# Optimization experiments

Hardware: AMD Instinct MI355X
Metric: run time of the kernel (lower is better)

Reference implementation:

```python
import jax, jax.numpy as jnp
import numpy as np

N_NODES = 25000
N_EDGES = 500000
ND, ED, G = 32, 19, 200


def _lrelu(x):
    return jax.nn.leaky_relu(x, 0.01)


def setup_inputs() -> dict:
    key = jax.random.key(0)
    ks = jax.random.split(key, 12)
    s = 0.05
    return {
        "node_feats": jax.random.normal(ks[0], (N_NODES, ND), jnp.float32),
        "edge_feats": jax.random.normal(ks[1], (N_EDGES, ED), jnp.float32),
        "src": jax.random.randint(ks[2], (N_EDGES,), 0, N_NODES),
        "dst": jax.random.randint(ks[3], (N_EDGES,), 0, N_NODES),
        "Wn": jax.random.normal(ks[4], (G, ND), jnp.float32) * s,
        "bn": jnp.zeros((G,), jnp.float32),
        "We1": jax.random.normal(ks[5], (G, ND + ED), jnp.float32) * s,
        "be1": jnp.zeros((G,), jnp.float32),
        "We2": jax.random.normal(ks[6], (1, 2 * G), jnp.float32) * s,
        "be2": jnp.zeros((1,), jnp.float32),
        "Wet": jax.random.normal(ks[7], (G, G), jnp.float32) * s,
        "bet": jnp.zeros((G,), jnp.float32),
        "W_ih": jax.random.normal(ks[8], (3 * G, G), jnp.float32) * s,
        "b_ih": jnp.zeros((3 * G,), jnp.float32),
        "W_hh": jax.random.normal(ks[9], (3 * G, G), jnp.float32) * s,
        "b_hh": jnp.zeros((3 * G,), jnp.float32),
    }


def reference(node_feats, edge_feats, src, dst, Wn, bn, We1, be1, We2, be2,
              Wet, bet, W_ih, b_ih, W_hh, b_hh):
    N = node_feats.shape[0]
    # project_node: Linear + LeakyReLU -> hv_new [N, G]
    hv_new = _lrelu(node_feats @ Wn.T + bn)
    # apply_edges1 + project_edge1: cat([src hv, he]) -> he1 [E, G]
    he1 = _lrelu(jnp.concatenate([node_feats[src], edge_feats], axis=1) @ We1.T + be1)
    # apply_edges2 + project_edge2: cat([dst hv_new, he1]) -> logits [E, 1]
    he2 = jnp.concatenate([hv_new[dst], he1], axis=1)
    logits = _lrelu(he2 @ We2.T + be2)[:, 0]  # [E]
    # edge_softmax: softmax over incoming edges per destination node
    m = jax.ops.segment_max(logits, dst, num_segments=N)  # [N]
    ex = jnp.exp(logits - m[dst])
    denom = jax.ops.segment_sum(ex, dst, num_segments=N)  # [N]
    a = ex / denom[dst]  # [E]
    # AttentiveGRU1: e = a * edge_transform(he1); scatter-sum to dst
    e = a[:, None] * (he1 @ Wet.T + bet)  # [E, G]
    c = jax.ops.segment_sum(e, dst, num_segments=N)  # [N, G]
    context = jax.nn.elu(c)
    # GRUCell(context, hv_new)
    gi = context @ W_ih.T + b_ih
    gh = hv_new @ W_hh.T + b_hh
    ir, iz, inn = jnp.split(gi, 3, axis=1)
    hr, hz, hn = jnp.split(gh, 3, axis=1)
    r = jax.nn.sigmoid(ir + hr)
    z = jax.nn.sigmoid(iz + hz)
    n = jnp.tanh(inn + r * hn)
    h = (1.0 - z) * n + z * hv_new
    return jax.nn.relu(h)
```

## Files before the change

kernel.cpp:

```cpp
#include <hip/hip_runtime.h>
#include <hip/hip_bf16.h>

#define G 200
#define NDIM 32
#define EDIM 19
#define KIN 51

typedef unsigned short u16;
typedef unsigned int u32;
typedef unsigned long long u64;

typedef __attribute__((ext_vector_type(8))) short bfrag;
typedef __attribute__((ext_vector_type(4))) float ffrag;

__device__ __forceinline__ float lrelu(float x){ return x > 0.f ? x : 0.01f*x; }
__device__ __forceinline__ u16 f2b(float x){ u32 u = __float_as_uint(x); return (u16)((u + 0x7fffu + ((u >> 16) & 1u)) >> 16); }
__device__ __forceinline__ float b2f(u16 x){ return __uint_as_float(((u32)x) << 16); }

#define MFMA16(a, b, c) __builtin_amdgcn_mfma_f32_16x16x32_bf16(a, b, c, 0, 0, 0)

__global__ void zero_kernel(float* __restrict__ s_raw, float* __restrict__ denom,
                            int* __restrict__ deg, float* __restrict__ l1,
                            const float* __restrict__ nf, u16* __restrict__ nfb, int N){
  int i = blockIdx.x * 256 + threadIdx.x;
  if (i < N * G) s_raw[i] = 0.f;
  if (i < N){ denom[i] = 0.f; deg[i] = 0; l1[i] = 0.f; }
  if (i < N * NDIM) nfb[i] = f2b(nf[i]);
}

__global__ void prep_all_kernel(const float* __restrict__ We1, const float* __restrict__ Wn,
                                const float* __restrict__ Wet, const float* __restrict__ Wih,
                                const float* __restrict__ Whh,
                                u16* __restrict__ Wbg, u16* __restrict__ Wnb, u16* __restrict__ Wet2,
                                u16* __restrict__ Wrz, u16* __restrict__ Winn, u16* __restrict__ Whn){
  int idx = blockIdx.x * 256 + threadIdx.x;
  const int s0 = 208 * 64, s1 = 256 * 64, s2 = 208 * 224, s3 = 2 * 208 * 416, s4 = 208 * 224, s5 = 208 * 224;
  if (idx < s0){
    int r = idx >> 6, k = idx & 63;
    Wbg[idx] = f2b((r < G && k < KIN) ? We1[r * KIN + k] : 0.f);
    return;
  }
  idx -= s0;
  if (idx < s1){
    int r = idx >> 6, k = idx & 63;
    Wnb[idx] = f2b((r < G && k < NDIM) ? Wn[r * NDIM + k] : 0.f);
    return;
  }
  idx -= s1;
  if (idx < s2){
    int r = idx / 224, k = idx % 224;
    Wet2[idx] = f2b((r < G && k < G) ? Wet[r * G + k] : 0.f);
    return;
  }
  idx -= s2;
  if (idx < s3){
    int g = idx / (208 * 416), rem = idx % (208 * 416);
    int r = rem / 416, k = rem % 416;
    float v = 0.f;
    if (r < G){
      int row = g * G + r;
      if (k < G) v = Wih[row * G + k];
      else if (k >= 208 && k < 408) v = Whh[row * G + (k - 208)];
    }
    Wrz[idx] = f2b(v);
    return;
  }
  idx -= s3;
  if (idx < s4){
    int r = idx / 224, k = idx % 224;
    Winn[idx] = f2b((r < G && k < G) ? Wih[(2 * G + r) * G + k] : 0.f);
    return;
  }
  idx -= s4;
  if (idx < s5){
    int r = idx / 224, kk = idx % 224;
    Whn[idx] = f2b((r < G && kk >= 16 && kk < 216) ? Whh[(2 * G + r) * G + (kk - 16)] : 0.f);
  }
}

__global__ void deghist_kernel(const int* __restrict__ dst, int* __restrict__ deg, int E){
  int e = blockIdx.x * 256 + threadIdx.x;
  if (e < E) atomicAdd(&deg[dst[e]], 1);
}

__global__ __launch_bounds__(1024) void scan_kernel(const int* __restrict__ deg, int* __restrict__ offs,
                                                    int* __restrict__ cur, int N){
  __shared__ int wsums[16];
  const int C = 25;
  int tid = threadIdx.x;
  int lane = tid & 63, wid = tid >> 6;
  int base = tid * C;
  int loc[C];
  int s = 0;
  #pragma unroll
  for (int i = 0; i < C; ++i){
    int v = (base + i < N) ? deg[base + i] : 0;
    loc[i] = s; s += v;
  }
  int x = s;
  #pragma unroll
  for (int off = 1; off < 64; off <<= 1){
    int y = __shfl_up(x, off, 64);
    if (lane >= off) x += y;
  }
  if (lane == 63) wsums[wid] = x;
  __syncthreads();
  if (wid == 0){
    int w = (lane < 16) ? wsums[lane] : 0;
    #pragma unroll
    for (int off = 1; off < 16; off <<= 1){
      int y = __shfl_up(w, off, 64);
      if (lane >= off) w += y;
    }
    if (lane < 16) wsums[lane] = w;
  }
  __syncthreads();
  int excl = ((wid ? wsums[wid - 1] : 0) + x) - s;
  #pragma unroll
  for (int i = 0; i < C; ++i){
    int o = excl + loc[i];
    if (base + i < N){ offs[base + i] = o; cur[base + i] = o; }
  }
  if (tid == 1023) offs[N] = excl + s;
}

__global__ void scatter_pack_kernel(const int* __restrict__ dst, const int* __restrict__ src,
                                    const float* __restrict__ ef,
                                    int* __restrict__ cur, int2* __restrict__ ds2,
                                    u16* __restrict__ efc, int E){
  int e = blockIdx.x * 256 + threadIdx.x;
  if (e >= E) return;
  int d = dst[e];
  int pos = atomicAdd(&cur[d], 1);
  ds2[pos] = make_int2(d, src[e]);
  const float* ep = ef + (long)e * EDIM;
  u32 w[12];
  #pragma unroll
  for (int j = 0; j < 12; ++j){
    int k0 = 2 * j, k1 = 2 * j + 1;
    u16 lo = (k0 < EDIM) ? f2b(ep[k0]) : (u16)0;
    u16 hi = (k1 < EDIM) ? f2b(ep[k1]) : (u16)0;
    w[j] = (u32)lo | ((u32)hi << 16);
  }
  uint4* dp = (uint4*)(efc + (long)pos * 24);
  dp[0] = make_uint4(w[0], w[1], w[2], w[3]);
  dp[1] = make_uint4(w[4], w[5], w[6], w[7]);
  dp[2] = make_uint4(w[8], w[9], w[10], w[11]);
}

__global__ __launch_bounds__(256) void hvgemm_kernel(
    const float* __restrict__ nf, const u16* __restrict__ Wnb, const float* __restrict__ bn,
    const float* __restrict__ We2, float* __restrict__ hv, float* __restrict__ l1, int M)
{
  __shared__ __align__(16) u16 As[64][72];
  __shared__ __align__(16) u16 Ws[64][72];
  int tid = threadIdx.x;
  int m0 = blockIdx.y * 64, n0 = blockIdx.x * 64;
  int l = tid & 63, w = tid >> 6, quad = l >> 4, col = l & 15;

  for (int idx = tid; idx < 64 * 16; idx += 256){
    int r = idx >> 4, c4 = idx & 15;
    int row = m0 + r, k = c4 * 4;
    float4 v = make_float4(0.f,0.f,0.f,0.f);
    if (row < M && k < NDIM) v = *(const float4*)(nf + (long)row * NDIM + k);
    *(ushort4*)&As[r][c4 * 4] = make_ushort4(f2b(v.x), f2b(v.y), f2b(v.z), f2b(v.w));
  }
  for (int idx = tid; idx < 64 * 8; idx += 256){
    int r = idx >> 3, c = idx & 7;
    *(ulonglong2*)&Ws[r][c * 8] = *(const ulonglong2*)(Wnb + (long)(n0 + r) * 64 + c * 8);
  }
  __syncthreads();
  bfrag a0 = *(const bfrag*)&As[w * 16 + col][quad * 8];
  bfrag a1 = *(const bfrag*)&As[w * 16 + col][32 + quad * 8];
  ffrag acc[4];
  #pragma unroll
  for (int t = 0; t < 4; ++t){ acc[t].x = 0.f; acc[t].y = 0.f; acc[t].z = 0.f; acc[t].w = 0.f; }
  #pragma unroll
  for (int t = 0; t < 4; ++t){
    bfrag b0 = *(const bfrag*)&Ws[t * 16 + col][quad * 8];
    bfrag b1 = *(const bfrag*)&Ws[t * 16 + col][32 + quad * 8];
    acc[t] = MFMA16(a0, b0, acc[t]);
    acc[t] = MFMA16(a1, b1, acc[t]);
  }
  float lp[4] = {0.f, 0.f, 0.f, 0.f};
  #pragma unroll
  for (int t = 0; t < 4; ++t){
    int n = n0 + t * 16 + col;
    float bv = (n < G) ? bn[n] : 0.f;
    float wv = (n < G) ? We2[n] : 0.f;
    #pragma unroll
    for (int r = 0; r < 4; ++r){
      int row = m0 + w * 16 + quad * 4 + r;
      float v = lrelu(acc[t][r] + bv);
      lp[r] += wv * v;
      if (n < G && row < M) hv[(long)row * G + n] = v;
    }
  }
  #pragma unroll
  for (int r = 0; r < 4; ++r){
    lp[r] += __shfl_xor(lp[r], 1, 16);
    lp[r] += __shfl_xor(lp[r], 2, 16);
    lp[r] += __shfl_xor(lp[r], 4, 16);
    lp[r] += __shfl_xor(lp[r], 8, 16);
  }
  if (col == 0){
    #pragma unroll
    for (int r = 0; r < 4; ++r){
      int row = m0 + w * 16 + quad * 4 + r;
      if (row < M) atomicAdd(&l1[row], lp[r]);
    }
  }
}

#define SST 72
__global__ __launch_bounds__(256) void edge_csr_kernel(
    const u16* __restrict__ nfb, const u16* __restrict__ efc,
    const int2* __restrict__ ds2, const int* __restrict__ offs,
    const u16* __restrict__ Wbg, const float* __restrict__ be1,
    const float* __restrict__ We2, const float* __restrict__ be2,
    const float* __restrict__ l1,
    float* __restrict__ s_raw, float* __restrict__ denom, int E)
{
  __shared__ __align__(16) u16 shm[208 * SST];
  __shared__ int segnode[64];
  __shared__ __align__(16) u16 exb[64];
  __shared__ __align__(8) unsigned char segb[64];
  __shared__ int Svar;

  int tid = threadIdx.x;
  int j0 = blockIdx.x * 64;
  int l = tid & 63, w = tid >> 6;
  int quad = l >> 4, col = l & 15;
  int m0 = w * 16;

  if (tid < 64){
    int j = j0 + tid;
    int valid = j < E;
    int n = valid ? ds2[j].x : -1;
    int nn = (tid == 63 || j + 1 >= E) ? -2 : ds2[j + 1].x;
    int f1 = (valid && n != nn) ? 1 : 0;
    int f2 = 0;
    if (f1 && offs[n] >= j0 && offs[n + 1] <= j0 + 64) f2 = 1;
    u64 em = __ballot(f1 != 0);
    int seg = (int)__popcll(em & ((1ull << tid) - 1ull));
    segb[tid] = (unsigned char)seg;
    if (f1) segnode[seg] = (n << 1) | f2;
    if (tid == 0) Svar = (int)__popcll(em);
    shm[200 * SST + tid] = 0x3F80;
  }

  int el = m0 + col;
  int j = j0 + el;
  bool vld = j < E;
  int srci = vld ? ds2[j].y : 0;
  bfrag a0 = {0,0,0,0,0,0,0,0};
  bfrag a1 = {0,0,0,0,0,0,0,0};
  if (vld){
    a0 = *(const bfrag*)(nfb + (long)srci * NDIM + quad * 8);
    if (quad < 3) a1 = *(const bfrag*)(efc + (long)j * 24 + quad * 8);
  }

  float pl[4] = {0.f, 0.f, 0.f, 0.f};
  #pragma unroll
  for (int t = 0; t < 13; ++t){
    bfrag b0 = *(const bfrag*)(Wbg + (t * 16 + col) * 64 + quad * 8);
    bfrag b1 = *(const bfrag*)(Wbg + (t * 16 + col) * 64 + 32 + quad * 8);
    ffrag acc; acc.x = 0.f; acc.y = 0.f; acc.z = 0.f; acc.w = 0.f;
    acc = MFMA16(a0, b0, acc);
    acc = MFMA16(a1, b1, acc);
    int g = t * 16 + col;
    float bv = (g < G) ? be1[g] : 0.f;
    float wv = (g < G) ? We2[G + g] : 0.f;
    float v0 = lrelu(acc.x + bv), v1 = lrelu(acc.y + bv);
    float v2 = lrelu(acc.z + bv), v3 = lrelu(acc.w + bv);
    pl[0] += wv * v0; pl[1] += wv * v1; pl[2] += wv * v2; pl[3] += wv * v3;
    if (g < G)
      *(ushort4*)&shm[g * SST + m0 + quad * 4] = make_ushort4(f2b(v0), f2b(v1), f2b(v2), f2b(v3));
  }
  #pragma unroll
  for (int r = 0; r < 4; ++r){
    pl[r] += __shfl_xor(pl[r], 1, 16);
    pl[r] += __shfl_xor(pl[r], 2, 16);
    pl[r] += __shfl_xor(pl[r], 4, 16);
    pl[r] += __shfl_xor(pl[r], 8, 16);
  }
  if (col == 0){
    #pragma unroll
    for (int r = 0; r < 4; ++r){
      int ee = m0 + quad * 4 + r;
      float ex = 0.f;
      if (j0 + ee < E){
        int n = ds2[j0 + ee].x;
        float lg = lrelu(pl[r] + l1[n] + be2[0]);
        ex = __expf(lg);
      }
      exb[ee] = f2b(ex);
    }
  }
  __syncthreads();

  int S = Svar;
  for (int mt = 0; mt * 16 < S; ++mt){
    int m = mt * 16 + col;
    u64 sb0 = *(const u64*)&segb[quad * 8];
    u64 sb1 = *(const u64*)&segb[32 + quad * 8];
    ulonglong2 ew0 = *(const ulonglong2*)&exb[quad * 8];
    ulonglong2 ew1 = *(const ulonglong2*)&exb[32 + quad * 8];
    bfrag A0, A1;
    #pragma unroll
    for (int jj = 0; jj < 8; ++jj){
      int s0i = (int)((sb0 >> (8 * jj)) & 0xFF);
      int s1i = (int)((sb1 >> (8 * jj)) & 0xFF);
      u64 w0 = (jj < 4) ? ew0.x : ew0.y;
      u64 w1 = (jj < 4) ? ew1.x : ew1.y;
      u16 e0 = (u16)(w0 >> (16 * (jj & 3)));
      u16 e1 = (u16)(w1 >> (16 * (jj & 3)));
      A0[jj] = (s0i == m) ? (short)e0 : (short)0;
      A1[jj] = (s1i == m) ? (short)e1 : (short)0;
    }
    int cnt = (w == 3) ? 4 : 3;
    for (int i = 0; i < cnt; ++i){
      int t = w * 3 + i;
      bfrag b0 = *(const bfrag*)&shm[(t * 16 + col) * SST + quad * 8];
      bfrag b1 = *(const bfrag*)&shm[(t * 16 + col) * SST + 32 + quad * 8];
      ffrag acc; acc.x = 0.f; acc.y = 0.f; acc.z = 0.f; acc.w = 0.f;
      acc = MFMA16(A0, b0, acc);
      acc = MFMA16(A1, b1, acc);
      int g = t * 16 + col;
      #pragma unroll
      for (int r = 0; r < 4; ++r){
        int seg = mt * 16 + quad * 4 + r;
        if (seg < S && g <= 200){
          int enc = segnode[seg];
          int nd = enc >> 1;
          float v = acc[r];
          float* pd = (g < G) ? (s_raw + (long)nd * G + g) : (denom + nd);
          if (enc & 1) *pd = v; else atomicAdd(pd, v);
        }
      }
    }
  }
}

#define XST 420
__global__ __launch_bounds__(256) void ctxgru_kernel(
    const float* __restrict__ s_raw, const float* __restrict__ hv, const float* __restrict__ denom,
    const u16* __restrict__ Wet2, const u16* __restrict__ Wrz,
    const u16* __restrict__ Winn, const u16* __restrict__ Whn,
    const float* __restrict__ bet, const float* __restrict__ b_ih, const float* __restrict__ b_hh,
    float* __restrict__ out, int M)
{
  __shared__ __align__(16) u16 X[64 * XST];
  __shared__ float invds[64];
  int tid = threadIdx.x;
  int m0 = blockIdx.x * 64;

  if (tid < 64){
    float dn = (m0 + tid < M) ? denom[m0 + tid] : 0.f;
    invds[tid] = dn > 0.f ? 1.f / dn : 0.f;
  }
  __syncthreads();

  for (int idx = tid; idx < 64 * 50; idx += 256){
    int r = idx / 50, c = idx % 50;
    int row = m0 + r;
    float4 v = make_float4(0.f,0.f,0.f,0.f), h = make_float4(0.f,0.f,0.f,0.f);
    if (row < M){
      v = *(const float4*)(s_raw + (long)row * G + c * 4);
      h = *(const float4*)(hv + (long)row * G + c * 4);
    }
    float iv = invds[r];
    *(ushort4*)&X[r * XST + c * 4] = make_ushort4(f2b(v.x*iv), f2b(v.y*iv), f2b(v.z*iv), f2b(v.w*iv));
    *(ushort4*)&X[r * XST + 208 + c * 4] = make_ushort4(f2b(h.x), f2b(h.y), f2b(h.z), f2b(h.w));
  }
  for (int idx = tid; idx < 64 * 4; idx += 256){
    int r = idx / 4, q = idx % 4;
    int base = (q < 2) ? (200 + q * 4) : (408 + (q - 2) * 4);
    *(ushort4*)&X[r * XST + base] = make_ushort4(0,0,0,0);
  }
  __syncthreads();

  int l = tid & 63, w = tid >> 6, quad = l >> 4, col = l & 15;
  int rowbase = w * 16;

  bfrag a1[7];
  #pragma unroll
  for (int j = 0; j < 7; ++j) a1[j] = *(const bfrag*)&X[(rowbase + col) * XST + j * 32 + quad * 8];

  for (int st = 0; st < 13; ++st){
    int n = st * 16 + col;
    ffrag acc; acc.x = 0.f; acc.y = 0.f; acc.z = 0.f; acc.w = 0.f;
    #pragma unroll
    for (int j = 0; j < 7; ++j){
      bfrag b = *(const bfrag*)(Wet2 + (long)n * 224 + j * 32 + quad * 8);
      acc = MFMA16(a1[j], b, acc);
    }
    if (n < G){
      float bv = bet[n];
      #pragma unroll
      for (int r = 0; r < 4; ++r){
        int lr = rowbase + quad * 4 + r;
        float gate = invds[lr] > 0.f ? 1.f : 0.f;
        float v = acc[r] + gate * bv;
        v = (v > 0.f) ? v : (__expf(v) - 1.f);
        X[lr * XST + n] = f2b(v);
      }
    }
  }
  __syncthreads();

  bfrag a2[13];
  #pragma unroll
  for (int j = 0; j < 13; ++j) a2[j] = *(const bfrag*)&X[(rowbase + col) * XST + j * 32 + quad * 8];

  for (int st = 0; st < 13; ++st){
    int n = st * 16 + col;
    ffrag ar, az, ai, ah;
    ar.x=ar.y=ar.z=ar.w=0.f; az.x=az.y=az.z=az.w=0.f;
    ai.x=ai.y=ai.z=ai.w=0.f; ah.x=ah.y=ah.z=ah.w=0.f;
    #pragma unroll
    for (int j = 0; j < 13; ++j){
      bfrag br_ = *(const bfrag*)(Wrz + (long)n * 416 + j * 32 + quad * 8);
      ar = MFMA16(a2[j], br_, ar);
      bfrag bz_ = *(const bfrag*)(Wrz + (long)(208 + n) * 416 + j * 32 + quad * 8);
      az = MFMA16(a2[j], bz_, az);
    }
    #pragma unroll
    for (int j = 0; j < 7; ++j){
      bfrag bi_ = *(const bfrag*)(Winn + (long)n * 224 + j * 32 + quad * 8);
      ai = MFMA16(a2[j], bi_, ai);
      bfrag bh_ = *(const bfrag*)(Whn + (long)n * 224 + j * 32 + quad * 8);
      ah = MFMA16(a2[j + 6], bh_, ah);
    }
    if (n < G){
      float br = b_ih[n] + b_hh[n];
      float bz = b_ih[G + n] + b_hh[G + n];
      float bi = b_ih[2 * G + n];
      float bh = b_hh[2 * G + n];
      #pragma unroll
      for (int r = 0; r < 4; ++r){
        int lr = rowbase + quad * 4 + r;
        int row = m0 + lr;
        if (row < M){
          float rg = 1.f / (1.f + __expf(-(ar[r] + br)));
          float zg = 1.f / (1.f + __expf(-(az[r] + bz)));
          float ng = tanhf(ai[r] + bi + rg * (ah[r] + bh));
          float hvv = b2f(X[lr * XST + 208 + n]);
          float h = (1.f - zg) * ng + zg * hvv;
          out[(long)row * G + n] = h > 0.f ? h : 0.f;
        }
      }
    }
  }
}

extern "C" void kernel_launch(void* const* d_in, const int* in_sizes, int n_in,
                              void* d_out, int out_size, void* d_ws, size_t ws_size,
                              hipStream_t stream)
{
  const float* nf   = (const float*)d_in[0];
  const float* ef   = (const float*)d_in[1];
  const int*   src  = (const int*)d_in[2];
  const int*   dst  = (const int*)d_in[3];
  const float* Wn   = (const float*)d_in[4];
  const float* bn   = (const float*)d_in[5];
  const float* We1  = (const float*)d_in[6];
  const float* be1  = (const float*)d_in[7];
  const float* We2  = (const float*)d_in[8];
  const float* be2  = (const float*)d_in[9];
  const float* Wet  = (const float*)d_in[10];
  const float* bet  = (const float*)d_in[11];
  const float* W_ih = (const float*)d_in[12];
  const float* b_ih = (const float*)d_in[13];
  const float* W_hh = (const float*)d_in[14];
  const float* b_hh = (const float*)d_in[15];
  int N = in_sizes[0] / NDIM;
  int E = in_sizes[2];
  float* out = (float*)d_out;

  char* p = (char*)d_ws;
  auto alloc = [&](size_t b){ char* r = p; p += (b + 255) & ~(size_t)255; return r; };
  float* hv    = (float*)alloc((size_t)N * G * 4);
  float* s_raw = (float*)alloc((size_t)N * G * 4);
  float* denom = (float*)alloc((size_t)N * 4);
  int*   deg   = (int*)  alloc((size_t)N * 4);
  int*   offs  = (int*)  alloc((size_t)(N + 1) * 4);
  int*   cur   = (int*)  alloc((size_t)N * 4);
  int2*  ds2   = (int2*) alloc((size_t)E * 8);
  u16*   efc   = (u16*)  alloc((size_t)E * 24 * 2);
  u16*   nfb   = (u16*)  alloc((size_t)N * NDIM * 2);
  float* l1    = (float*)alloc((size_t)N * 4);
  u16*   Wbg   = (u16*)  alloc((size_t)208 * 64 * 2);
  u16*   Wnb   = (u16*)  alloc((size_t)256 * 64 * 2);
  u16*   Wet2  = (u16*)  alloc((size_t)208 * 224 * 2);
  u16*   Wrz   = (u16*)  alloc((size_t)2 * 208 * 416 * 2);
  u16*   Winn  = (u16*)  alloc((size_t)208 * 224 * 2);
  u16*   Whn   = (u16*)  alloc((size_t)208 * 224 * 2);

  int eb = (E + 255) / 256;
  int mb = (N + 63) / 64;
  const int prep_total = 208*64 + 256*64 + 208*224 + 2*208*416 + 208*224 + 208*224;

  zero_kernel<<<dim3((N * G + 255) / 256), dim3(256), 0, stream>>>(s_raw, denom, deg, l1, nf, nfb, N);
  prep_all_kernel<<<dim3((prep_total + 255) / 256), dim3(256), 0, stream>>>(
      We1, Wn, Wet, W_ih, W_hh, Wbg, Wnb, Wet2, Wrz, Winn, Whn);
  deghist_kernel<<<dim3(eb), dim3(256), 0, stream>>>(dst, deg, E);
  scan_kernel<<<dim3(1), dim3(1024), 0, stream>>>(deg, offs, cur, N);
  scatter_pack_kernel<<<dim3(eb), dim3(256), 0, stream>>>(dst, src, ef, cur, ds2, efc, E);
  hvgemm_kernel<<<dim3(4, mb), dim3(256), 0, stream>>>(nf, Wnb, bn, We2, hv, l1, N);
  edge_csr_kernel<<<dim3((E + 63) / 64), dim3(256), 0, stream>>>(nfb, efc, ds2, offs,
                                                                 Wbg, be1, We2, be2, l1, s_raw, denom, E);
  ctxgru_kernel<<<dim3(mb), dim3(256), 0, stream>>>(s_raw, hv, denom, Wet2, Wrz, Winn, Whn,
                                                    bet, b_ih, b_hh, out, N);
}
```

Baseline: 449.3 us.

## Pack per-edge records with dst, src, l1 and features; merge init kernels

After: 450.9 us. Within noise of the previous version (+0.4%).

```diff
diff --git a/kernel.cpp b/kernel.cpp
--- a/kernel.cpp
+++ b/kernel.cpp
@@ -19,21 +19,20 @@
 
 #define MFMA16(a, b, c) __builtin_amdgcn_mfma_f32_16x16x32_bf16(a, b, c, 0, 0, 0)
 
-__global__ void zero_kernel(float* __restrict__ s_raw, float* __restrict__ denom,
+__global__ void init_kernel(float* __restrict__ s_raw, float* __restrict__ denom,
                             int* __restrict__ deg, float* __restrict__ l1,
-                            const float* __restrict__ nf, u16* __restrict__ nfb, int N){
+                            const float* __restrict__ nf, u16* __restrict__ nfb,
+                            const float* __restrict__ We1, const float* __restrict__ Wn,
+                            const float* __restrict__ Wet, const float* __restrict__ Wih,
+                            const float* __restrict__ Whh,
+                            u16* __restrict__ Wbg, u16* __restrict__ Wnb, u16* __restrict__ Wet2,
+                            u16* __restrict__ Wrz, u16* __restrict__ Winn, u16* __restrict__ Whn, int N){
   int i = blockIdx.x * 256 + threadIdx.x;
   if (i < N * G) s_raw[i] = 0.f;
   if (i < N){ denom[i] = 0.f; deg[i] = 0; l1[i] = 0.f; }
   if (i < N * NDIM) nfb[i] = f2b(nf[i]);
-}
-
-__global__ void prep_all_kernel(const float* __restrict__ We1, const float* __restrict__ Wn,
-                                const float* __restrict__ Wet, const float* __restrict__ Wih,
-                                const float* __restrict__ Whh,
-                                u16* __restrict__ Wbg, u16* __restrict__ Wnb, u16* __restrict__ Wet2,
-                                u16* __restrict__ Wrz, u16* __restrict__ Winn, u16* __restrict__ Whn){
-  int idx = blockIdx.x * 256 + threadIdx.x;
+
+  int idx = i;
   const int s0 = 208 * 64, s1 = 256 * 64, s2 = 208 * 224, s3 = 2 * 208 * 416, s4 = 208 * 224, s5 = 208 * 224;
   if (idx < s0){
     int r = idx >> 6, k = idx & 63;
@@ -85,18 +84,29 @@
 
 __global__ __launch_bounds__(1024) void scan_kernel(const int* __restrict__ deg, int* __restrict__ offs,
                                                     int* __restrict__ cur, int N){
+  __shared__ int sd[12800];
   __shared__ int wsums[16];
   const int C = 25;
   int tid = threadIdx.x;
   int lane = tid & 63, wid = tid >> 6;
-  int base = tid * C;
-  int loc[C];
+  int val[C];
+  for (int h = 0; h < 2; ++h){
+    int base_h = h * 12800;
+    for (int k = tid; k < 12800; k += 1024){
+      int gi = base_h + k;
+      sd[k] = (gi < N) ? deg[gi] : 0;
+    }
+    __syncthreads();
+    if ((tid >> 9) == h){
+      int t0 = (tid - h * 512) * C;
+      #pragma unroll
+      for (int i = 0; i < C; ++i) val[i] = sd[t0 + i];
+    }
+    __syncthreads();
+  }
   int s = 0;
   #pragma unroll
-  for (int i = 0; i < C; ++i){
-    int v = (base + i < N) ? deg[base + i] : 0;
-    loc[i] = s; s += v;
-  }
+  for (int i = 0; i < C; ++i){ int v = val[i]; val[i] = s; s += v; }
   int x = s;
   #pragma unroll
   for (int off = 1; off < 64; off <<= 1){
@@ -116,36 +126,37 @@
   }
   __syncthreads();
   int excl = ((wid ? wsums[wid - 1] : 0) + x) - s;
+  int base = tid * C;
   #pragma unroll
   for (int i = 0; i < C; ++i){
-    int o = excl + loc[i];
+    int o = excl + val[i];
     if (base + i < N){ offs[base + i] = o; cur[base + i] = o; }
   }
   if (tid == 1023) offs[N] = excl + s;
 }
 
 __global__ void scatter_pack_kernel(const int* __restrict__ dst, const int* __restrict__ src,
-                                    const float* __restrict__ ef,
-                                    int* __restrict__ cur, int2* __restrict__ ds2,
-                                    u16* __restrict__ efc, int E){
+                                    const float* __restrict__ ef, const float* __restrict__ l1,
+                                    int* __restrict__ cur, u32* __restrict__ erec, int E){
   int e = blockIdx.x * 256 + threadIdx.x;
   if (e >= E) return;
   int d = dst[e];
   int pos = atomicAdd(&cur[d], 1);
-  ds2[pos] = make_int2(d, src[e]);
+  u32 w[16];
+  w[0] = (u32)d; w[1] = (u32)src[e]; w[2] = __float_as_uint(l1[d]); w[3] = 0u;
   const float* ep = ef + (long)e * EDIM;
-  u32 w[12];
   #pragma unroll
   for (int j = 0; j < 12; ++j){
     int k0 = 2 * j, k1 = 2 * j + 1;
     u16 lo = (k0 < EDIM) ? f2b(ep[k0]) : (u16)0;
     u16 hi = (k1 < EDIM) ? f2b(ep[k1]) : (u16)0;
-    w[j] = (u32)lo | ((u32)hi << 16);
-  }
-  uint4* dp = (uint4*)(efc + (long)pos * 24);
+    w[4 + j] = (u32)lo | ((u32)hi << 16);
+  }
+  uint4* dp = (uint4*)(erec + (size_t)pos * 16);
   dp[0] = make_uint4(w[0], w[1], w[2], w[3]);
   dp[1] = make_uint4(w[4], w[5], w[6], w[7]);
   dp[2] = make_uint4(w[8], w[9], w[10], w[11]);
+  dp[3] = make_uint4(w[12], w[13], w[14], w[15]);
 }
 
 __global__ __launch_bounds__(256) void hvgemm_kernel(
@@ -214,11 +225,9 @@
 
 #define SST 72
 __global__ __launch_bounds__(256) void edge_csr_kernel(
-    const u16* __restrict__ nfb, const u16* __restrict__ efc,
-    const int2* __restrict__ ds2, const int* __restrict__ offs,
+    const u16* __restrict__ nfb, const u32* __restrict__ erec, const int* __restrict__ offs,
     const u16* __restrict__ Wbg, const float* __restrict__ be1,
     const float* __restrict__ We2, const float* __restrict__ be2,
-    const float* __restrict__ l1,
     float* __restrict__ s_raw, float* __restrict__ denom, int E)
 {
   __shared__ __align__(16) u16 shm[208 * SST];
@@ -236,8 +245,8 @@
   if (tid < 64){
     int j = j0 + tid;
     int valid = j < E;
-    int n = valid ? ds2[j].x : -1;
-    int nn = (tid == 63 || j + 1 >= E) ? -2 : ds2[j + 1].x;
+    int n = valid ? (int)erec[(size_t)j * 16] : -1;
+    int nn = (tid == 63 || j + 1 >= E) ? -2 : (int)erec[(size_t)(j + 1) * 16];
     int f1 = (valid && n != nn) ? 1 : 0;
     int f2 = 0;
     if (f1 && offs[n] >= j0 && offs[n + 1] <= j0 + 64) f2 = 1;
@@ -252,12 +261,12 @@
   int el = m0 + col;
   int j = j0 + el;
   bool vld = j < E;
-  int srci = vld ? ds2[j].y : 0;
+  int srci = vld ? (int)erec[(size_t)j * 16 + 1] : 0;
   bfrag a0 = {0,0,0,0,0,0,0,0};
   bfrag a1 = {0,0,0,0,0,0,0,0};
   if (vld){
     a0 = *(const bfrag*)(nfb + (long)srci * NDIM + quad * 8);
-    if (quad < 3) a1 = *(const bfrag*)(efc + (long)j * 24 + quad * 8);
+    if (quad < 3) a1 = *(const bfrag*)((const u16*)erec + (size_t)j * 32 + 8 + quad * 8);
   }
 
   float pl[4] = {0.f, 0.f, 0.f, 0.f};
@@ -290,8 +299,8 @@
       int ee = m0 + quad * 4 + r;
       float ex = 0.f;
       if (j0 + ee < E){
-        int n = ds2[j0 + ee].x;
-        float lg = lrelu(pl[r] + l1[n] + be2[0]);
+        float l1v = __uint_as_float(erec[(size_t)(j0 + ee) * 16 + 2]);
+        float lg = lrelu(pl[r] + l1v + be2[0]);
         ex = __expf(lg);
       }
       exb[ee] = f2b(ex);
@@ -486,8 +495,7 @@
   int*   deg   = (int*)  alloc((size_t)N * 4);
   int*   offs  = (int*)  alloc((size_t)(N + 1) * 4);
   int*   cur   = (int*)  alloc((size_t)N * 4);
-  int2*  ds2   = (int2*) alloc((size_t)E * 8);
-  u16*   efc   = (u16*)  alloc((size_t)E * 24 * 2);
+  u32*   erec  = (u32*)  alloc((size_t)E * 64);
   u16*   nfb   = (u16*)  alloc((size_t)N * NDIM * 2);
   float* l1    = (float*)alloc((size_t)N * 4);
   u16*   Wbg   = (u16*)  alloc((size_t)208 * 64 * 2);
@@ -499,17 +507,16 @@
 
   int eb = (E + 255) / 256;
   int mb = (N + 63) / 64;
-  const int prep_total = 208*64 + 256*64 + 208*224 + 2*208*416 + 208*224 + 208*224;
-
-  zero_kernel<<<dim3((N * G + 255) / 256), dim3(256), 0, stream>>>(s_raw, denom, deg, l1, nf, nfb, N);
-  prep_all_kernel<<<dim3((prep_total + 255) / 256), dim3(256), 0, stream>>>(
-      We1, Wn, Wet, W_ih, W_hh, Wbg, Wnb, Wet2, Wrz, Winn, Whn);
+
+  init_kernel<<<dim3((N * G + 255) / 256), dim3(256), 0, stream>>>(
+      s_raw, denom, deg, l1, nf, nfb, We1, Wn, Wet, W_ih, W_hh,
+      Wbg, Wnb, Wet2, Wrz, Winn, Whn, N);
   deghist_kernel<<<dim3(eb), dim3(256), 0, stream>>>(dst, deg, E);
   scan_kernel<<<dim3(1), dim3(1024), 0, stream>>>(deg, offs, cur, N);
-  scatter_pack_kernel<<<dim3(eb), dim3(256), 0, stream>>>(dst, src, ef, cur, ds2, efc, E);
   hvgemm_kernel<<<dim3(4, mb), dim3(256), 0, stream>>>(nf, Wnb, bn, We2, hv, l1, N);
-  edge_csr_kernel<<<dim3((E + 63) / 64), dim3(256), 0, stream>>>(nfb, efc, ds2, offs,
-                                                                 Wbg, be1, We2, be2, l1, s_raw, denom, E);
+  scatter_pack_kernel<<<dim3(eb), dim3(256), 0, stream>>>(dst, src, ef, l1, cur, erec, E);
+  edge_csr_kernel<<<dim3((E + 63) / 64), dim3(256), 0, stream>>>(nfb, erec, offs,
+                                                                 Wbg, be1, We2, be2, s_raw, denom, E);
   ctxgru_kernel<<<dim3(mb), dim3(256), 0, stream>>>(s_raw, hv, denom, Wet2, Wrz, Winn, Whn,
                                                     bet, b_ih, b_hh, out, N);
 }
```
